# Performance work log

Hardware: AMD Instinct MI355X
Metric: run time of the kernel (lower is better)

Reference implementation:

```python
import jax, jax.numpy as jnp
import numpy as np

B, CQ, CK, CV, CO = 16, 256, 256, 256, 256
H, W = 80, 80          # query spatial size (P3-like)
KH, KW = 40, 40        # key/value spatial size (P4-like)
HEADS = 4
R2 = 2 * 2             # region_size ** 2
SCALE = 1.0 / np.float32(np.sqrt(CQ))


def conv1x1(x, w, b):
    # 1x1 conv == per-pixel linear map over channels
    return jnp.einsum('bchw,oc->bohw', x, w) + b[None, :, None, None]


def setup_inputs() -> dict:
    key = jax.random.key(0)
    ks = jax.random.split(key, 10)
    s = 0.05
    return {
        'query': jax.random.normal(ks[0], (B, CQ, H, W), jnp.float32),
        'key':   jax.random.normal(ks[1], (B, CK, KH, KW), jnp.float32),
        'wq': jax.random.normal(ks[2], (CQ, CQ), jnp.float32) * s,
        'bq': jax.random.normal(ks[3], (CQ,), jnp.float32) * s,
        'wk': jax.random.normal(ks[4], (CK, CK), jnp.float32) * s,
        'bk': jax.random.normal(ks[5], (CK,), jnp.float32) * s,
        'wv': jax.random.normal(ks[6], (CV, CV), jnp.float32) * s,
        'bv': jax.random.normal(ks[7], (CV,), jnp.float32) * s,
        'wo': jax.random.normal(ks[8], (CO, CV), jnp.float32) * s,
        'bo': jax.random.normal(ks[9], (CO,), jnp.float32) * s,
    }


def reference(query, key, wq, bq, wk, bk, wv, bv, wo, bo):
    # value defaults to key in the original module
    q = conv1x1(query, wq, bq)               # [B,CQ,H,W]
    k = conv1x1(key, wk, bk)                 # [B,CK,KH,KW]
    v = conv1x1(key, wv, bv)                 # [B,CV,KH,KW]

    b, cq, h, w = q.shape
    # All R2 'patches' in the source are the SAME interpolation (no offsets),
    # so compute it once; bilinear resize matches torch align_corners=False.
    ki = jax.image.resize(k, (b, k.shape[1], h, w), method='bilinear')
    vi = jax.image.resize(v, (b, v.shape[1], h, w), method='bilinear')

    q5 = q.reshape(b, HEADS, cq // HEADS, h, w)
    k5 = ki.reshape(b, HEADS, k.shape[1] // HEADS, h, w)
    v5 = vi.reshape(b, HEADS, v.shape[1] // HEADS, h, w)

    # per-region score; identical for every region patch
    score = jnp.einsum('bhcxy,bhcxy->bhxy', q5, k5) * SCALE     # [B,h,H,W]
    scores = jnp.broadcast_to(score[:, :, None], (b, HEADS, R2, h, w))
    # NOTE: original uses nn.Softmax(dim=3) -> normalizes over the H axis
    attn = jax.nn.softmax(scores, axis=3)                       # [B,h,R2,H,W]

    # out = sum over regions of attn * v (v identical across regions)
    out = jnp.einsum('bhrxy,bhcxy->bhcxy', attn, v5)            # [B,h,C/h,H,W]
    out = out.reshape(b, -1, h, w)                              # [B,CV,H,W]
    return conv1x1(out, wo, bo)                                 # [B,CO,H,W]
```

## Files before the change

kernel.cpp:

```cpp
#include <hip/hip_runtime.h>
#include <hip/hip_bf16.h>

typedef __bf16 bf16;
typedef __attribute__((ext_vector_type(4))) float f32x4;
typedef __attribute__((ext_vector_type(8))) __bf16 bf16x8;
typedef __attribute__((ext_vector_type(4))) __bf16 bf16x4;

__global__ __launch_bounds__(256, 2)
void gemm_cm(const float* __restrict__ act, const float* __restrict__ W,
             const float* __restrict__ bias, bf16* __restrict__ out, int P) {
  __shared__ alignas(16) bf16 At[128][64];
  __shared__ alignas(16) bf16 Bt[128][64];
  const int t = threadIdx.x;
  const int b = blockIdx.z;
  const int m0 = blockIdx.x * 128;
  const int n0 = blockIdx.y * 128;
  const int w = t >> 6, l = t & 63;
  const int wr = w >> 1, wc = w & 1;
  const int lrow = l & 15, koff = (l >> 4) * 8;

  const float* actb = act + (size_t)b * 256 * (size_t)P;

  f32x4 acc[4][4];
#pragma unroll
  for (int i = 0; i < 4; ++i)
#pragma unroll
    for (int j = 0; j < 4; ++j) acc[i][j] = (f32x4){0.f, 0.f, 0.f, 0.f};

  for (int kt = 0; kt < 4; ++kt) {
    const int k0 = kt * 64;
    if (kt) __syncthreads();
#pragma unroll
    for (int u = 0; u < 2; ++u) {
      int unit = u * 256 + t;
      int up = unit & 31;
      int uk = unit >> 5;
      int ps = m0 + up * 4;
      if (ps > P - 4) ps = P - 4;
      f32x4 r0 = *(const f32x4*)(actb + (size_t)(k0 + uk * 4 + 0) * P + ps);
      f32x4 r1 = *(const f32x4*)(actb + (size_t)(k0 + uk * 4 + 1) * P + ps);
      f32x4 r2 = *(const f32x4*)(actb + (size_t)(k0 + uk * 4 + 2) * P + ps);
      f32x4 r3 = *(const f32x4*)(actb + (size_t)(k0 + uk * 4 + 3) * P + ps);
      int cs = (uk * 4) ^ ((up & 7) << 3);
#pragma unroll
      for (int j = 0; j < 4; ++j) {
        bf16x4 v = {(bf16)r0[j], (bf16)r1[j], (bf16)r2[j], (bf16)r3[j]};
        *(bf16x4*)&At[up * 4 + j][cs] = v;
      }
    }
#pragma unroll
    for (int it = 0; it < 8; ++it) {
      int idx = it * 256 + t;
      int row = idx >> 4, ce = (idx & 15) * 4;
      f32x4 v = *(const f32x4*)(W + (size_t)(n0 + row) * 256 + k0 + ce);
      bf16x4 h = {(bf16)v[0], (bf16)v[1], (bf16)v[2], (bf16)v[3]};
      *(bf16x4*)&Bt[row][ce] = h;
    }
    __syncthreads();

#pragma unroll
    for (int kk = 0; kk < 2; ++kk) {
      bf16x8 af[4], bv[4];
#pragma unroll
      for (int i = 0; i < 4; ++i) {
        int ar = wr * 64 + i * 16 + lrow;
        int kb = kk * 32 + koff;
        af[i] = *(const bf16x8*)&At[ar][kb ^ (((ar >> 2) & 7) << 3)];
        bv[i] = *(const bf16x8*)&Bt[wc * 64 + i * 16 + lrow][kb];
      }
#pragma unroll
      for (int mi = 0; mi < 4; ++mi)
#pragma unroll
        for (int ni = 0; ni < 4; ++ni)
          acc[mi][ni] = __builtin_amdgcn_mfma_f32_16x16x32_bf16(af[mi], bv[ni], acc[mi][ni], 0, 0, 0);
    }
  }

  bf16* ob = out + (size_t)b * (size_t)P * 256;
#pragma unroll
  for (int mi = 0; mi < 4; ++mi) {
#pragma unroll
    for (int r = 0; r < 4; ++r) {
      int p_ = m0 + wr * 64 + mi * 16 + (l >> 4) * 4 + r;
      if (p_ < P) {
#pragma unroll
        for (int ni = 0; ni < 4; ++ni) {
          int o_ = n0 + wc * 64 + ni * 16 + (l & 15);
          ob[(size_t)p_ * 256 + o_] = (bf16)(acc[mi][ni][r] + bias[o_]);
        }
      }
    }
  }
}

__global__ __launch_bounds__(256, 2)
void gemm_pm(const bf16* __restrict__ act, const float* __restrict__ W,
             const float* __restrict__ bias, float* __restrict__ out, int P) {
  __shared__ alignas(16) bf16 At[128][64];
  __shared__ alignas(16) bf16 Bt[128][64];
  const int t = threadIdx.x;
  const int b = blockIdx.z;
  const int m0 = blockIdx.x * 128;
  const int n0 = blockIdx.y * 128;
  const int w = t >> 6, l = t & 63;
  const int wr = w >> 1, wc = w & 1;
  const int lrow = l & 15, koff = (l >> 4) * 8;

  const bf16* actb = act + (size_t)b * (size_t)P * 256;

  f32x4 acc[4][4];
#pragma unroll
  for (int i = 0; i < 4; ++i)
#pragma unroll
    for (int j = 0; j < 4; ++j) acc[i][j] = (f32x4){0.f, 0.f, 0.f, 0.f};

  for (int kt = 0; kt < 4; ++kt) {
    const int k0 = kt * 64;
    if (kt) __syncthreads();
#pragma unroll
    for (int it = 0; it < 8; ++it) {
      int idx = it * 256 + t;
      int row = idx >> 4, ce = (idx & 15) * 4;
      f32x4 v = *(const f32x4*)(W + (size_t)(m0 + row) * 256 + k0 + ce);
      bf16x4 h = {(bf16)v[0], (bf16)v[1], (bf16)v[2], (bf16)v[3]};
      *(bf16x4*)&At[row][ce] = h;
    }
#pragma unroll
    for (int it = 0; it < 4; ++it) {
      int idx = it * 256 + t;
      int row = idx >> 3, ce = (idx & 7) * 8;
      bf16x8 v = *(const bf16x8*)(actb + (size_t)(n0 + row) * 256 + k0 + ce);
      *(bf16x8*)&Bt[row][ce] = v;
    }
    __syncthreads();

#pragma unroll
    for (int kk = 0; kk < 2; ++kk) {
      bf16x8 af[4], bv[4];
#pragma unroll
      for (int i = 0; i < 4; ++i) {
        af[i] = *(const bf16x8*)&At[wr * 64 + i * 16 + lrow][kk * 32 + koff];
        bv[i] = *(const bf16x8*)&Bt[wc * 64 + i * 16 + lrow][kk * 32 + koff];
      }
#pragma unroll
      for (int mi = 0; mi < 4; ++mi)
#pragma unroll
        for (int ni = 0; ni < 4; ++ni)
          acc[mi][ni] = __builtin_amdgcn_mfma_f32_16x16x32_bf16(af[mi], bv[ni], acc[mi][ni], 0, 0, 0);
    }
  }

  float* ob = out + (size_t)b * 256 * (size_t)P;
#pragma unroll
  for (int mi = 0; mi < 4; ++mi) {
#pragma unroll
    for (int r = 0; r < 4; ++r) {
      int o_ = m0 + wr * 64 + mi * 16 + (l >> 4) * 4 + r;
      float bvf = bias[o_];
#pragma unroll
      for (int ni = 0; ni < 4; ++ni) {
        int p_ = n0 + wc * 64 + ni * 16 + (l & 15);
        ob[(size_t)o_ * P + p_] = acc[mi][ni][r] + bvf;
      }
    }
  }
}

__global__ void score_kernel(const bf16* __restrict__ Qpm, const bf16* __restrict__ Kpm,
                             float* __restrict__ score) {
  const int t = threadIdx.x;
  const int p = blockIdx.x * 256 + t;
  const int hd = blockIdx.y, b = blockIdx.z;
  const int x = p / 80, y = p % 80;

  float cx = 0.5f * x - 0.25f;
  int ix = (int)floorf(cx);
  float wx1 = cx - ix;
  int x0 = ix < 0 ? 0 : ix, x1 = (ix + 1 > 39) ? 39 : ix + 1;
  float cy = 0.5f * y - 0.25f;
  int iy = (int)floorf(cy);
  float wy1 = cy - iy;
  int y0 = iy < 0 ? 0 : iy, y1 = (iy + 1 > 39) ? 39 : iy + 1;
  float w00 = (1.f - wx1) * (1.f - wy1), w01 = (1.f - wx1) * wy1;
  float w10 = wx1 * (1.f - wy1), w11 = wx1 * wy1;

  const bf16* q   = Qpm + ((size_t)b * 6400 + p) * 256 + hd * 64;
  const bf16* k00 = Kpm + ((size_t)b * 1600 + x0 * 40 + y0) * 256 + hd * 64;
  const bf16* k01 = Kpm + ((size_t)b * 1600 + x0 * 40 + y1) * 256 + hd * 64;
  const bf16* k10 = Kpm + ((size_t)b * 1600 + x1 * 40 + y0) * 256 + hd * 64;
  const bf16* k11 = Kpm + ((size_t)b * 1600 + x1 * 40 + y1) * 256 + hd * 64;

  float dot = 0.f;
#pragma unroll
  for (int i = 0; i < 8; ++i) {
    bf16x8 qv = *(const bf16x8*)(q + i * 8);
    bf16x8 a = *(const bf16x8*)(k00 + i * 8);
    bf16x8 c = *(const bf16x8*)(k01 + i * 8);
    bf16x8 d = *(const bf16x8*)(k10 + i * 8);
    bf16x8 e = *(const bf16x8*)(k11 + i * 8);
#pragma unroll
    for (int j = 0; j < 8; ++j) {
      float kup = w00 * (float)a[j] + w01 * (float)c[j] + w10 * (float)d[j] + w11 * (float)e[j];
      dot += (float)qv[j] * kup;
    }
  }
  score[((size_t)b * 4 + hd) * 6400 + p] = dot * 0.0625f;
}

__global__ void smax_kernel(float* __restrict__ score) {
  __shared__ float s[6400];
  const int hd = blockIdx.x, b = blockIdx.y, t = threadIdx.x;
  float* buf = score + ((size_t)b * 4 + hd) * 6400;
  for (int i = t; i < 6400; i += 256) s[i] = buf[i];
  __syncthreads();
  if (t < 80) {
    const int y = t;
    float m = -1e30f;
    for (int x = 0; x < 80; ++x) m = fmaxf(m, s[x * 80 + y]);
    float sum = 0.f;
    for (int x = 0; x < 80; ++x) {
      float e = __expf(s[x * 80 + y] - m);
      s[x * 80 + y] = e;
      sum += e;
    }
    float inv = 4.0f / sum;
    for (int x = 0; x < 80; ++x) buf[x * 80 + y] = s[x * 80 + y] * inv;
  }
}

__global__ void outgen_kernel(const bf16* __restrict__ Vpm, const float* __restrict__ attn,
                              bf16* __restrict__ outpm) {
  __shared__ float Vx[40][256];
  __shared__ float at[4][80];
  const int x = blockIdx.x, b = blockIdx.y, t = threadIdx.x;

  float cx = 0.5f * x - 0.25f;
  int ix = (int)floorf(cx);
  float wx1 = cx - ix, wx0 = 1.f - wx1;
  int tx0 = ix < 0 ? 0 : ix, tx1 = (ix + 1 > 39) ? 39 : ix + 1;

  const bf16* r0 = Vpm + ((size_t)b * 1600 + tx0 * 40) * 256;
  const bf16* r1 = Vpm + ((size_t)b * 1600 + tx1 * 40) * 256;
  for (int ty = 0; ty < 40; ++ty)
    Vx[ty][t] = wx0 * (float)r0[ty * 256 + t] + wx1 * (float)r1[ty * 256 + t];
  for (int i = t; i < 320; i += 256) {
    int hd = i / 80, y = i % 80;
    at[hd][y] = attn[((size_t)b * 4 + hd) * 6400 + x * 80 + y];
  }
  __syncthreads();

  const int hd = t >> 6;
  bf16* ob = outpm + ((size_t)b * 6400 + x * 80) * 256;
  for (int y = 0; y < 80; ++y) {
    float cyv = 0.5f * y - 0.25f;
    int iy = (int)floorf(cyv);
    float wy1 = cyv - iy;
    int ty0 = iy < 0 ? 0 : iy, ty1 = (iy + 1 > 39) ? 39 : iy + 1;
    float v = (1.f - wy1) * Vx[ty0][t] + wy1 * Vx[ty1][t];
    ob[(size_t)y * 256 + t] = (bf16)(at[hd][y] * v);
  }
}

extern "C" void kernel_launch(void* const* d_in, const int* in_sizes, int n_in,
                              void* d_out, int out_size, void* d_ws, size_t ws_size,
                              hipStream_t stream) {
  const float* query = (const float*)d_in[0];
  const float* key   = (const float*)d_in[1];
  const float* wq    = (const float*)d_in[2];
  const float* bq    = (const float*)d_in[3];
  const float* wk    = (const float*)d_in[4];
  const float* bk    = (const float*)d_in[5];
  const float* wv    = (const float*)d_in[6];
  const float* bv    = (const float*)d_in[7];
  const float* wo    = (const float*)d_in[8];
  const float* bo    = (const float*)d_in[9];

  char* ws = (char*)d_ws;
  bf16*  outpm = (bf16*)(ws);
  bf16*  Kpm   = (bf16*)(ws + 52428800);
  bf16*  Vpm   = (bf16*)(ws + 65536000);
  float* score = (float*)(ws + 78643200);
  bf16*  Qpm   = (bf16*)d_out;

  gemm_cm<<<dim3(50, 2, 16), 256, 0, stream>>>(query, wq, bq, Qpm, 6400);
  gemm_cm<<<dim3(13, 2, 16), 256, 0, stream>>>(key, wk, bk, Kpm, 1600);
  gemm_cm<<<dim3(13, 2, 16), 256, 0, stream>>>(key, wv, bv, Vpm, 1600);
  score_kernel<<<dim3(25, 4, 16), 256, 0, stream>>>(Qpm, Kpm, score);
  smax_kernel<<<dim3(4, 16), 256, 0, stream>>>(score);
  outgen_kernel<<<dim3(80, 16), 256, 0, stream>>>(Vpm, score, outpm);
  gemm_pm<<<dim3(2, 50, 16), 256, 0, stream>>>(outpm, wo, bo, (float*)d_out, 6400);
}
```

Before: 208.5 us.

## Double-buffer GEMM LDS tiles with register prefetch and merge K/V projections

Both GEMM kernels now stage tiles through two LDS buffers. The next k-tile's global loads go into registers while the MFMAs work on the current buffer, which removes one barrier per iteration and hides load latency. The K and V 1x1-conv projections, which read the same key tensor, are merged into one launch that selects weights by blockIdx.y. The LDS swizzle is also changed to XOR on row&7 for both operands. In exchange, the doubled LDS and the extra prefetch registers may lower occupancy.

```diff
diff --git a/kernel.cpp b/kernel.cpp
--- a/kernel.cpp
+++ b/kernel.cpp
@@ -7,10 +7,132 @@
 typedef __attribute__((ext_vector_type(4))) __bf16 bf16x4;
 
 __global__ __launch_bounds__(256, 2)
-void gemm_cm(const float* __restrict__ act, const float* __restrict__ W,
-             const float* __restrict__ bias, bf16* __restrict__ out, int P) {
-  __shared__ alignas(16) bf16 At[128][64];
-  __shared__ alignas(16) bf16 Bt[128][64];
+void gemm_cm(const float* __restrict__ act,
+             const float* __restrict__ W0, const float* __restrict__ b0, bf16* __restrict__ out0,
+             const float* __restrict__ W1, const float* __restrict__ b1, bf16* __restrict__ out1,
+             int P) {
+  __shared__ alignas(16) bf16 At[2][128][64];
+  __shared__ alignas(16) bf16 Bt[2][128][64];
+  const int t = threadIdx.x;
+  const int b = blockIdx.z;
+  const int m0 = blockIdx.x * 128;
+  const int sel = blockIdx.y >> 1;
+  const int n0 = (blockIdx.y & 1) * 128;
+  const float* W    = sel ? W1 : W0;
+  const float* bias = sel ? b1 : b0;
+  bf16*        out  = sel ? out1 : out0;
+
+  const int w = t >> 6, l = t & 63;
+  const int wr = w >> 1, wc = w & 1;
+  const int lrow = l & 15, koff = (l >> 4) * 8;
+
+  const float* actb = act + (size_t)b * 256 * (size_t)P;
+
+  f32x4 Ar[2][4];
+  f32x4 Br[8];
+
+  auto LOAD = [&](int kt) {
+    const int k0 = kt * 64;
+#pragma unroll
+    for (int u = 0; u < 2; ++u) {
+      int unit = u * 256 + t;
+      int up = unit & 31, uk = unit >> 5;
+      int ps = m0 + up * 4;
+      if (ps > P - 4) ps = P - 4;
+#pragma unroll
+      for (int j = 0; j < 4; ++j)
+        Ar[u][j] = *(const f32x4*)(actb + (size_t)(k0 + uk * 4 + j) * P + ps);
+    }
+#pragma unroll
+    for (int it = 0; it < 8; ++it) {
+      int idx = it * 256 + t;
+      int row = idx >> 4, ce = (idx & 15) * 4;
+      Br[it] = *(const f32x4*)(W + (size_t)(n0 + row) * 256 + k0 + ce);
+    }
+  };
+
+  auto STORE = [&](int buf) {
+#pragma unroll
+    for (int u = 0; u < 2; ++u) {
+      int unit = u * 256 + t;
+      int up = unit & 31, uk = unit >> 5;
+#pragma unroll
+      for (int j = 0; j < 4; ++j) {
+        int row = up * 4 + j;
+        int cs = (uk * 4) ^ ((row & 7) << 3);
+        bf16x4 v = {(bf16)Ar[u][0][j], (bf16)Ar[u][1][j], (bf16)Ar[u][2][j], (bf16)Ar[u][3][j]};
+        *(bf16x4*)&At[buf][row][cs] = v;
+      }
+    }
+#pragma unroll
+    for (int it = 0; it < 8; ++it) {
+      int idx = it * 256 + t;
+      int row = idx >> 4, ce = (idx & 15) * 4;
+      int cs = ce ^ ((row & 7) << 3);
+      bf16x4 h = {(bf16)Br[it][0], (bf16)Br[it][1], (bf16)Br[it][2], (bf16)Br[it][3]};
+      *(bf16x4*)&Bt[buf][row][cs] = h;
+    }
+  };
+
+  f32x4 acc[4][4];
+#pragma unroll
+  for (int i = 0; i < 4; ++i)
+#pragma unroll
+    for (int j = 0; j < 4; ++j) acc[i][j] = (f32x4){0.f, 0.f, 0.f, 0.f};
+
+  auto COMPUTE = [&](int buf) {
+#pragma unroll
+    for (int kk = 0; kk < 2; ++kk) {
+      bf16x8 af[4], bv[4];
+      const int kb = kk * 32 + koff;
+#pragma unroll
+      for (int i = 0; i < 4; ++i) {
+        int ar = wr * 64 + i * 16 + lrow;
+        int br = wc * 64 + i * 16 + lrow;
+        af[i] = *(const bf16x8*)&At[buf][ar][kb ^ ((ar & 7) << 3)];
+        bv[i] = *(const bf16x8*)&Bt[buf][br][kb ^ ((br & 7) << 3)];
+      }
+#pragma unroll
+      for (int mi = 0; mi < 4; ++mi)
+#pragma unroll
+        for (int ni = 0; ni < 4; ++ni)
+          acc[mi][ni] = __builtin_amdgcn_mfma_f32_16x16x32_bf16(af[mi], bv[ni], acc[mi][ni], 0, 0, 0);
+    }
+  };
+
+  LOAD(0);
+  STORE(0);
+  __syncthreads();
+#pragma unroll
+  for (int kt = 0; kt < 4; ++kt) {
+    if (kt < 3) LOAD(kt + 1);
+    COMPUTE(kt & 1);
+    if (kt < 3) STORE((kt + 1) & 1);
+    __syncthreads();
+  }
+
+  bf16* ob = out + (size_t)b * (size_t)P * 256;
+#pragma unroll
+  for (int mi = 0; mi < 4; ++mi) {
+#pragma unroll
+    for (int r = 0; r < 4; ++r) {
+      int p_ = m0 + wr * 64 + mi * 16 + (l >> 4) * 4 + r;
+      if (p_ < P) {
+#pragma unroll
+        for (int ni = 0; ni < 4; ++ni) {
+          int o_ = n0 + wc * 64 + ni * 16 + (l & 15);
+          ob[(size_t)p_ * 256 + o_] = (bf16)(acc[mi][ni][r] + bias[o_]);
+        }
+      }
+    }
+  }
+}
+
+__global__ __launch_bounds__(256, 2)
+void gemm_pm(const bf16* __restrict__ act, const float* __restrict__ W,
+             const float* __restrict__ bias, float* __restrict__ out, int P) {
+  __shared__ alignas(16) bf16 At[2][128][64];
+  __shared__ alignas(16) bf16 Bt[2][128][64];
   const int t = threadIdx.x;
   const int b = blockIdx.z;
   const int m0 = blockIdx.x * 128;
@@ -19,7 +141,44 @@
   const int wr = w >> 1, wc = w & 1;
   const int lrow = l & 15, koff = (l >> 4) * 8;
 
-  const float* actb = act + (size_t)b * 256 * (size_t)P;
+  const bf16* actb = act + (size_t)b * (size_t)P * 256;
+
+  f32x4 Ar[8];
+  bf16x8 Brr[4];
+
+  auto LOAD = [&](int kt) {
+    const int k0 = kt * 64;
+#pragma unroll
+    for (int it = 0; it < 8; ++it) {
+      int idx = it * 256 + t;
+      int row = idx >> 4, ce = (idx & 15) * 4;
+      Ar[it] = *(const f32x4*)(W + (size_t)(m0 + row) * 256 + k0 + ce);
+    }
+#pragma unroll
+    for (int it = 0; it < 4; ++it) {
+      int idx = it * 256 + t;
+      int row = idx >> 3, ce = (idx & 7) * 8;
+      Brr[it] = *(const bf16x8*)(actb + (size_t)(n0 + row) * 256 + k0 + ce);
+    }
+  };
+
+  auto STORE = [&](int buf) {
+#pragma unroll
+    for (int it = 0; it < 8; ++it) {
+      int idx = it * 256 + t;
+      int row = idx >> 4, ce = (idx & 15) * 4;
+      int cs = ce ^ ((row & 7) << 3);
+      bf16x4 h = {(bf16)Ar[it][0], (bf16)Ar[it][1], (bf16)Ar[it][2], (bf16)Ar[it][3]};
+      *(bf16x4*)&At[buf][row][cs] = h;
+    }
+#pragma unroll
+    for (int it = 0; it < 4; ++it) {
+      int idx = it * 256 + t;
+      int row = idx >> 3, ce = (idx & 7) * 8;
+      int cs = ce ^ ((row & 7) << 3);
+      *(bf16x8*)&Bt[buf][row][cs] = Brr[it];
+    }
+  };
 
   f32x4 acc[4][4];
 #pragma unroll
@@ -27,46 +186,17 @@
 #pragma unroll
     for (int j = 0; j < 4; ++j) acc[i][j] = (f32x4){0.f, 0.f, 0.f, 0.f};
 
-  for (int kt = 0; kt < 4; ++kt) {
-    const int k0 = kt * 64;
-    if (kt) __syncthreads();
-#pragma unroll
-    for (int u = 0; u < 2; ++u) {
-      int unit = u * 256 + t;
-      int up = unit & 31;
-      int uk = unit >> 5;
-      int ps = m0 + up * 4;
-      if (ps > P - 4) ps = P - 4;
-      f32x4 r0 = *(const f32x4*)(actb + (size_t)(k0 + uk * 4 + 0) * P + ps);
-      f32x4 r1 = *(const f32x4*)(actb + (size_t)(k0 + uk * 4 + 1) * P + ps);
-      f32x4 r2 = *(const f32x4*)(actb + (size_t)(k0 + uk * 4 + 2) * P + ps);
-      f32x4 r3 = *(const f32x4*)(actb + (size_t)(k0 + uk * 4 + 3) * P + ps);
-      int cs = (uk * 4) ^ ((up & 7) << 3);
-#pragma unroll
-      for (int j = 0; j < 4; ++j) {
-        bf16x4 v = {(bf16)r0[j], (bf16)r1[j], (bf16)r2[j], (bf16)r3[j]};
-        *(bf16x4*)&At[up * 4 + j][cs] = v;
-      }
-    }
-#pragma unroll
-    for (int it = 0; it < 8; ++it) {
-      int idx = it * 256 + t;
-      int row = idx >> 4, ce = (idx & 15) * 4;
-      f32x4 v = *(const f32x4*)(W + (size_t)(n0 + row) * 256 + k0 + ce);
-      bf16x4 h = {(bf16)v[0], (bf16)v[1], (bf16)v[2], (bf16)v[3]};
-      *(bf16x4*)&Bt[row][ce] = h;
-    }
-    __syncthreads();
-
+  auto COMPUTE = [&](int buf) {
 #pragma unroll
     for (int kk = 0; kk < 2; ++kk) {
       bf16x8 af[4], bv[4];
+      const int kb = kk * 32 + koff;
 #pragma unroll
       for (int i = 0; i < 4; ++i) {
         int ar = wr * 64 + i * 16 + lrow;
-        int kb = kk * 32 + koff;
-        af[i] = *(const bf16x8*)&At[ar][kb ^ (((ar >> 2) & 7) << 3)];
-        bv[i] = *(const bf16x8*)&Bt[wc * 64 + i * 16 + lrow][kb];
+        int br = wc * 64 + i * 16 + lrow;
+        af[i] = *(const bf16x8*)&At[buf][ar][kb ^ ((ar & 7) << 3)];
+        bv[i] = *(const bf16x8*)&Bt[buf][br][kb ^ ((br & 7) << 3)];
       }
 #pragma unroll
       for (int mi = 0; mi < 4; ++mi)
@@ -74,80 +204,17 @@
         for (int ni = 0; ni < 4; ++ni)
           acc[mi][ni] = __builtin_amdgcn_mfma_f32_16x16x32_bf16(af[mi], bv[ni], acc[mi][ni], 0, 0, 0);
     }
-  }
-
-  bf16* ob = out + (size_t)b * (size_t)P * 256;
-#pragma unroll
-  for (int mi = 0; mi < 4; ++mi) {
-#pragma unroll
-    for (int r = 0; r < 4; ++r) {
-      int p_ = m0 + wr * 64 + mi * 16 + (l >> 4) * 4 + r;
-      if (p_ < P) {
-#pragma unroll
-        for (int ni = 0; ni < 4; ++ni) {
-          int o_ = n0 + wc * 64 + ni * 16 + (l & 15);
-          ob[(size_t)p_ * 256 + o_] = (bf16)(acc[mi][ni][r] + bias[o_]);
-        }
-      }
-    }
-  }
-}
-
-__global__ __launch_bounds__(256, 2)
-void gemm_pm(const bf16* __restrict__ act, const float* __restrict__ W,
-             const float* __restrict__ bias, float* __restrict__ out, int P) {
-  __shared__ alignas(16) bf16 At[128][64];
-  __shared__ alignas(16) bf16 Bt[128][64];
-  const int t = threadIdx.x;
-  const int b = blockIdx.z;
-  const int m0 = blockIdx.x * 128;
-  const int n0 = blockIdx.y * 128;
-  const int w = t >> 6, l = t & 63;
-  const int wr = w >> 1, wc = w & 1;
-  const int lrow = l & 15, koff = (l >> 4) * 8;
-
-  const bf16* actb = act + (size_t)b * (size_t)P * 256;
-
-  f32x4 acc[4][4];
-#pragma unroll
-  for (int i = 0; i < 4; ++i)
-#pragma unroll
-    for (int j = 0; j < 4; ++j) acc[i][j] = (f32x4){0.f, 0.f, 0.f, 0.f};
-
+  };
+
+  LOAD(0);
+  STORE(0);
+  __syncthreads();
+#pragma unroll
   for (int kt = 0; kt < 4; ++kt) {
-    const int k0 = kt * 64;
-    if (kt) __syncthreads();
-#pragma unroll
-    for (int it = 0; it < 8; ++it) {
-      int idx = it * 256 + t;
-      int row = idx >> 4, ce = (idx & 15) * 4;
-      f32x4 v = *(const f32x4*)(W + (size_t)(m0 + row) * 256 + k0 + ce);
-      bf16x4 h = {(bf16)v[0], (bf16)v[1], (bf16)v[2], (bf16)v[3]};
-      *(bf16x4*)&At[row][ce] = h;
-    }
-#pragma unroll
-    for (int it = 0; it < 4; ++it) {
-      int idx = it * 256 + t;
-      int row = idx >> 3, ce = (idx & 7) * 8;
-      bf16x8 v = *(const bf16x8*)(actb + (size_t)(n0 + row) * 256 + k0 + ce);
-      *(bf16x8*)&Bt[row][ce] = v;
-    }
+    if (kt < 3) LOAD(kt + 1);
+    COMPUTE(kt & 1);
+    if (kt < 3) STORE((kt + 1) & 1);
     __syncthreads();
-
-#pragma unroll
-    for (int kk = 0; kk < 2; ++kk) {
-      bf16x8 af[4], bv[4];
-#pragma unroll
-      for (int i = 0; i < 4; ++i) {
-        af[i] = *(const bf16x8*)&At[wr * 64 + i * 16 + lrow][kk * 32 + koff];
-        bv[i] = *(const bf16x8*)&Bt[wc * 64 + i * 16 + lrow][kk * 32 + koff];
-      }
-#pragma unroll
-      for (int mi = 0; mi < 4; ++mi)
-#pragma unroll
-        for (int ni = 0; ni < 4; ++ni)
-          acc[mi][ni] = __builtin_amdgcn_mfma_f32_16x16x32_bf16(af[mi], bv[ni], acc[mi][ni], 0, 0, 0);
-    }
   }
 
   float* ob = out + (size_t)b * 256 * (size_t)P;
@@ -282,9 +349,8 @@
   float* score = (float*)(ws + 78643200);
   bf16*  Qpm   = (bf16*)d_out;
 
-  gemm_cm<<<dim3(50, 2, 16), 256, 0, stream>>>(query, wq, bq, Qpm, 6400);
-  gemm_cm<<<dim3(13, 2, 16), 256, 0, stream>>>(key, wk, bk, Kpm, 1600);
-  gemm_cm<<<dim3(13, 2, 16), 256, 0, stream>>>(key, wv, bv, Vpm, 1600);
+  gemm_cm<<<dim3(50, 2, 16), 256, 0, stream>>>(query, wq, bq, Qpm, wq, bq, Qpm, 6400);
+  gemm_cm<<<dim3(13, 4, 16), 256, 0, stream>>>(key, wk, bk, Kpm, wv, bv, Vpm, 1600);
   score_kernel<<<dim3(25, 4, 16), 256, 0, stream>>>(Qpm, Kpm, score);
   smax_kernel<<<dim3(4, 16), 256, 0, stream>>>(score);
   outgen_kernel<<<dim3(80, 16), 256, 0, stream>>>(Vpm, score, outpm);
```

Measured after the change: 202.0 us. -3.1%, faster.
